# Optimization experiments

Measured on AMD Instinct MI355X. Metric: run time of the kernel, lower is better.

## Reference

```python
import jax, jax.numpy as jnp
import numpy as np

D_MODEL = 512
NUM_HEADS = 8
DEPTH = D_MODEL // NUM_HEADS


def setup_inputs() -> dict:
    key = jax.random.key(0)
    ks = jax.random.split(key, 11)
    B, S = 2, 4096
    scale = 1.0 / np.sqrt(D_MODEL)
    inp = {
        "q": jax.random.normal(ks[0], (B, S, D_MODEL), jnp.float32),
        "k": jax.random.normal(ks[1], (B, S, D_MODEL), jnp.float32),
        "v": jax.random.normal(ks[2], (B, S, D_MODEL), jnp.float32),
        "wq_w": jax.random.normal(ks[3], (D_MODEL, D_MODEL), jnp.float32) * scale,
        "wq_b": jnp.zeros((D_MODEL,), jnp.float32),
        "wk_w": jax.random.normal(ks[4], (D_MODEL, D_MODEL), jnp.float32) * scale,
        "wk_b": jnp.zeros((D_MODEL,), jnp.float32),
        "wv_w": jax.random.normal(ks[5], (D_MODEL, D_MODEL), jnp.float32) * scale,
        "wv_b": jnp.zeros((D_MODEL,), jnp.float32),
        "wo_w": jax.random.normal(ks[6], (D_MODEL, D_MODEL), jnp.float32) * scale,
        "wo_b": jnp.zeros((D_MODEL,), jnp.float32),
    }
    return inp


def _split_heads(x):
    # [B, S, D] -> [B, H, S, depth]
    B, S, _ = x.shape
    return x.reshape(B, S, NUM_HEADS, DEPTH).transpose(0, 2, 1, 3)


def reference(q, k, v, wq_w, wq_b, wk_w, wk_b, wv_w, wv_b, wo_w, wo_b):
    B, S, _ = q.shape
    qh = _split_heads(q @ wq_w.T + wq_b)  # [B,H,S,d]
    kh = _split_heads(k @ wk_w.T + wk_b)
    vh = _split_heads(v @ wv_w.T + wv_b)
    logits = jnp.einsum('bhqd,bhkd->bhqk', qh, kh) / jnp.sqrt(
        jnp.asarray(DEPTH, jnp.float32))
    attn = jax.nn.softmax(logits, axis=-1)
    out = jnp.einsum('bhqk,bhkd->bhqd', attn, vh)  # [B,H,S,d]
    out = out.transpose(0, 2, 1, 3).reshape(B, S, D_MODEL)
    return out @ wo_w.T + wo_b
```

## Files before the change

kernel.cpp:

```cpp
#include <hip/hip_runtime.h>

typedef __attribute__((ext_vector_type(8))) short short8;
typedef __attribute__((ext_vector_type(4))) float float4v;

#define D_MODEL 512
#define NUM_HEADS 8
#define DEPTH 64
#define SEQ 4096
#define BATCH 2
#define MROWS 8192
#define WSZ (D_MODEL * D_MODEL)
#define SCALE_Q 0.18033688011112043f

#define SW(r, c) (((r) * 64) + ((((c) ^ ((r) & 7))) * 8))

static __device__ __forceinline__ unsigned short f2bf(float f) {
  unsigned int u = __builtin_bit_cast(unsigned int, f);
  u += 0x7FFFu + ((u >> 16) & 1u);
  return (unsigned short)(u >> 16);
}
static __device__ __forceinline__ unsigned int pk2(float a, float b) {
  return (unsigned int)f2bf(a) | ((unsigned int)f2bf(b) << 16);
}
static __device__ __forceinline__ unsigned int pk2f(float a, float b) {
  unsigned int ua = __builtin_bit_cast(unsigned int, a) + 0x8000u;
  unsigned int ub = __builtin_bit_cast(unsigned int, b) + 0x8000u;
  return __builtin_amdgcn_perm(ub, ua, 0x07060302u);
}
static __device__ __forceinline__ short8 cvt8(const float* p) {
  float4v f0 = *(const float4v*)p;
  float4v f1 = *(const float4v*)(p + 4);
  short8 s;
#pragma unroll
  for (int j = 0; j < 4; ++j) {
    s[j] = (short)f2bf(f0[j]);
    s[4 + j] = (short)f2bf(f1[j]);
  }
  return s;
}

__global__ __launch_bounds__(256) void cvt3(const float* __restrict__ w0,
                                            const float* __restrict__ w1,
                                            const float* __restrict__ w2,
                                            unsigned short* __restrict__ dst) {
  const float* srcs[3] = {w0, w1, w2};
  const int z = blockIdx.y;
  const float4v* s = (const float4v*)srcs[z];
  uint2* d = (uint2*)(dst + (size_t)z * WSZ);
  int i = blockIdx.x * 256 + threadIdx.x;
  float4v f = s[i];
  d[i] = make_uint2(pk2(f[0], f[1]), pk2(f[2], f[3]));
}
__global__ __launch_bounds__(256) void cvt1(const float* __restrict__ w,
                                            unsigned short* __restrict__ dst) {
  int i = blockIdx.x * 256 + threadIdx.x;
  float4v f = ((const float4v*)w)[i];
  ((uint2*)dst)[i] = make_uint2(pk2(f[0], f[1]), pk2(f[2], f[3]));
}

struct QkvB {
  const float* X[3];
  const float* bias[3];
  unsigned short* out[3];
};
__global__ __launch_bounds__(256, 2) void qkv_fulln(QkvB a,
                                                    const unsigned short* __restrict__ Wall) {
  __shared__ unsigned short Xs[64 * 64];
  __shared__ unsigned short Ws[512 * 64];
  const int z = blockIdx.y;
  const float* __restrict__ X = a.X[z];
  const unsigned short* __restrict__ W = Wall + (size_t)z * WSZ;
  const float* __restrict__ bias = a.bias[z];
  unsigned short* __restrict__ out = a.out[z];
  const int t = threadIdx.x;
  const int w = t >> 6, l = t & 63, lq = l >> 4, lm = l & 15;
  const int mBase = blockIdx.x * 64;
  float4v acc[4][8] = {};

  for (int kc = 0; kc < D_MODEL; kc += 64) {
    __syncthreads();
#pragma unroll
    for (int p = 0; p < 2; ++p) {
      int i = p * 256 + t, r = i >> 3, c = i & 7;
      *(short8*)&Xs[SW(r, c)] = cvt8(&X[(size_t)(mBase + r) * D_MODEL + kc + c * 8]);
    }
#pragma unroll 4
    for (int p = 0; p < 16; ++p) {
      int i = p * 256 + t, r = i >> 3, c = i & 7;
      *(short8*)&Ws[SW(r, c)] = *(const short8*)&W[(size_t)r * D_MODEL + kc + c * 8];
    }
    __syncthreads();
#pragma unroll
    for (int kk = 0; kk < 2; ++kk) {
      short8 av[4];
#pragma unroll
      for (int fm = 0; fm < 4; ++fm)
        av[fm] = *(const short8*)&Xs[SW(fm * 16 + lm, kk * 4 + lq)];
#pragma unroll
      for (int fn = 0; fn < 8; ++fn) {
        short8 bv = *(const short8*)&Ws[SW(w * 128 + fn * 16 + lm, kk * 4 + lq)];
#pragma unroll
        for (int fm = 0; fm < 4; ++fm)
          acc[fm][fn] = __builtin_amdgcn_mfma_f32_16x16x32_bf16(av[fm], bv, acc[fm][fn], 0, 0, 0);
      }
    }
  }
  const int bb = mBase >> 12, s0 = mBase & 4095;
  if (z == 2) {
    __syncthreads();
    unsigned short* T = Ws;
#pragma unroll
    for (int fn = 0; fn < 8; ++fn) {
      int n = w * 128 + fn * 16 + lm;
      float bv = bias[n];
#pragma unroll
      for (int fm = 0; fm < 4; ++fm) {
        int m0 = fm * 16 + lq * 4;
        uint2 u;
        u.x = pk2(acc[fm][fn][0] + bv, acc[fm][fn][1] + bv);
        u.y = pk2(acc[fm][fn][2] + bv, acc[fm][fn][3] + bv);
        *(uint2*)&T[SW(n, m0 >> 3) + (lq & 1) * 4] = u;
      }
    }
    __syncthreads();
#pragma unroll
    for (int p = 0; p < 16; ++p) {
      int i = p * 256 + t, n = i >> 3, cm = i & 7;
      int h = n >> 6, d = n & 63;
      *(short8*)&out[(((size_t)(bb * NUM_HEADS + h) * DEPTH + d) << 12) + s0 + cm * 8] =
          *(const short8*)&T[SW(n, cm)];
    }
  } else {
    const float scale = (z == 0) ? SCALE_Q : 1.0f;
#pragma unroll
    for (int fn = 0; fn < 8; ++fn) {
      int gn = w * 128 + fn * 16 + lm;
      float bv = bias[gn];
      int h = gn >> 6, d = gn & 63;
#pragma unroll
      for (int fm = 0; fm < 4; ++fm) {
#pragma unroll
        for (int r = 0; r < 4; ++r) {
          int s = s0 + fm * 16 + lq * 4 + r;
          out[(((size_t)(bb * NUM_HEADS + h) * SEQ + s) << 6) + d] =
              f2bf((acc[fm][fn][r] + bv) * scale);
        }
      }
    }
  }
}

__global__ __launch_bounds__(256) void gemm_out_128x64(
    const unsigned short* __restrict__ X,
    const unsigned short* __restrict__ W,
    const float* __restrict__ bias,
    float* __restrict__ out) {
  __shared__ unsigned short As[128 * 64];
  __shared__ unsigned short Bs[64 * 64];
  const int t = threadIdx.x;
  const int w = t >> 6, l = t & 63, lq = l >> 4, lm = l & 15;
  const int mq = w * 32;
  const int mBase = blockIdx.x * 128, nBase = blockIdx.y * 64;
  float4v acc[2][4] = {};
  for (int kc = 0; kc < D_MODEL; kc += 64) {
    __syncthreads();
#pragma unroll
    for (int p = 0; p < 4; ++p) {
      int i = p * 256 + t, r = i >> 3, c = i & 7;
      *(short8*)&As[SW(r, c)] = *(const short8*)&X[(size_t)(mBase + r) * D_MODEL + kc + c * 8];
    }
#pragma unroll
    for (int p = 0; p < 2; ++p) {
      int i = p * 256 + t, r = i >> 3, c = i & 7;
      *(short8*)&Bs[SW(r, c)] = *(const short8*)&W[(size_t)(nBase + r) * D_MODEL + kc + c * 8];
    }
    __syncthreads();
#pragma unroll
    for (int kk = 0; kk < 2; ++kk) {
      short8 av[2];
#pragma unroll
      for (int fm = 0; fm < 2; ++fm)
        av[fm] = *(const short8*)&As[SW(mq + fm * 16 + lm, kk * 4 + lq)];
#pragma unroll
      for (int fn = 0; fn < 4; ++fn) {
        short8 bv = *(const short8*)&Bs[SW(fn * 16 + lm, kk * 4 + lq)];
#pragma unroll
        for (int fm = 0; fm < 2; ++fm)
          acc[fm][fn] = __builtin_amdgcn_mfma_f32_16x16x32_bf16(av[fm], bv, acc[fm][fn], 0, 0, 0);
      }
    }
  }
#pragma unroll
  for (int fn = 0; fn < 4; ++fn) {
    int gn = nBase + fn * 16 + lm;
    float bv = bias[gn];
#pragma unroll
    for (int fm = 0; fm < 2; ++fm) {
#pragma unroll
      for (int r = 0; r < 4; ++r) {
        int gm = mBase + mq + fm * 16 + lq * 4 + r;
        out[(size_t)gm * D_MODEL + gn] = acc[fm][fn][r] + bv;
      }
    }
  }
}

__global__ __launch_bounds__(256, 4) void attn(
    const unsigned short* __restrict__ Qh,
    const unsigned short* __restrict__ Kh,
    const unsigned short* __restrict__ Vt,
    unsigned short* __restrict__ AO)
{
  __shared__ unsigned short Ksub[2][64 * 64];
  __shared__ unsigned short Vsub[2][64 * 64];
  __shared__ unsigned short Psub[64 * 64];
  const int t = threadIdx.x;
  const int w = t >> 6;
  const int l = t & 63, lq = l >> 4, lm = l & 15;
  const int bh = blockIdx.y;
  const size_t base = (size_t)bh * SEQ * DEPTH;
  const int qbase = blockIdx.x * 64 + w * 16;
  const unsigned short* __restrict__ Kp = Kh + base;
  const unsigned short* __restrict__ Vp = Vt + base;

  short8 qf[2];
#pragma unroll
  for (int kk = 0; kk < 2; ++kk)
    qf[kk] = *(const short8*)&Qh[base + (size_t)(qbase + lm) * DEPTH + kk * 32 + lq * 8];

  short8 ones;
#pragma unroll
  for (int j = 0; j < 8; ++j) ones[j] = (short)0x3F80;

  float4v oacc[4] = {};
  float4v sumacc = {};
  short8 kreg[2], vreg[2];

#pragma unroll
  for (int p = 0; p < 2; ++p) {
    int i = p * 256 + t, r = i >> 3, c = i & 7;
    kreg[p] = *(const short8*)&Kp[(size_t)r * DEPTH + c * 8];
    vreg[p] = *(const short8*)&Vp[(size_t)r * SEQ + c * 8];
  }
#pragma unroll
  for (int p = 0; p < 2; ++p) {
    int i = p * 256 + t, r = i >> 3, c = i & 7;
    *(short8*)&Ksub[0][SW(r, c)] = kreg[p];
    *(short8*)&Vsub[0][SW(r, c)] = vreg[p];
  }
  __syncthreads();

  auto step = [&](int cur, int tile, bool pf) {
    if (pf) {
      const int s0n = (tile + 1) * 64;
#pragma unroll
      for (int p = 0; p < 2; ++p) {
        int i = p * 256 + t, r = i >> 3, c = i & 7;
        kreg[p] = *(const short8*)&Kp[(size_t)(s0n + r) * DEPTH + c * 8];
        vreg[p] = *(const short8*)&Vp[(size_t)r * SEQ + s0n + c * 8];
      }
    }
#pragma unroll
    for (int f = 0; f < 4; ++f) {
      float4v sacc = {};
#pragma unroll
      for (int kk = 0; kk < 2; ++kk) {
        short8 a = *(const short8*)&Ksub[cur][SW(f * 16 + lm, kk * 4 + lq)];
        sacc = __builtin_amdgcn_mfma_f32_16x16x32_bf16(a, qf[kk], sacc, 0, 0, 0);
      }
      uint2 u;
      u.x = pk2f(__builtin_amdgcn_exp2f(sacc[0]), __builtin_amdgcn_exp2f(sacc[1]));
      u.y = pk2f(__builtin_amdgcn_exp2f(sacc[2]), __builtin_amdgcn_exp2f(sacc[3]));
      *(uint2*)&Psub[SW(w * 16 + lm, 2 * f + (lq >> 1)) + (lq & 1) * 4] = u;
    }
#pragma unroll
    for (int kk = 0; kk < 2; ++kk) {
      short8 a0 = *(const short8*)&Psub[SW(w * 16 + lm, kk * 4 + lq)];
      sumacc = __builtin_amdgcn_mfma_f32_16x16x32_bf16(a0, ones, sumacc, 0, 0, 0);
#pragma unroll
      for (int df = 0; df < 4; ++df) {
        short8 b = *(const short8*)&Vsub[cur][SW(df * 16 + lm, kk * 4 + lq)];
        oacc[df] = __builtin_amdgcn_mfma_f32_16x16x32_bf16(a0, b, oacc[df], 0, 0, 0);
      }
    }
    if (pf) {
#pragma unroll
      for (int p = 0; p < 2; ++p) {
        int i = p * 256 + t, r = i >> 3, c = i & 7;
        *(short8*)&Ksub[cur ^ 1][SW(r, c)] = kreg[p];
        *(short8*)&Vsub[cur ^ 1][SW(r, c)] = vreg[p];
      }
    }
    __syncthreads();
  };

  for (int it = 0; it < 64; it += 2) {
    step(0, it, true);
    step(1, it + 1, it + 2 < 64);
  }

  const int bb = bh >> 3, h = bh & 7;
#pragma unroll
  for (int r = 0; r < 4; ++r) {
    float rinv = 1.0f / sumacc[r];
    int s = qbase + lq * 4 + r;
#pragma unroll
    for (int df = 0; df < 4; ++df) {
      int d = df * 16 + lm;
      AO[((size_t)(bb * SEQ + s)) * D_MODEL + h * DEPTH + d] = f2bf(oacc[df][r] * rinv);
    }
  }
}

extern "C" void kernel_launch(void* const* d_in, const int* in_sizes, int n_in,
                              void* d_out, int out_size, void* d_ws, size_t ws_size,
                              hipStream_t stream) {
  const float* q = (const float*)d_in[0];
  const float* k = (const float*)d_in[1];
  const float* v = (const float*)d_in[2];
  const float* wq = (const float*)d_in[3];
  const float* bq = (const float*)d_in[4];
  const float* wk = (const float*)d_in[5];
  const float* bk = (const float*)d_in[6];
  const float* wv = (const float*)d_in[7];
  const float* bv = (const float*)d_in[8];
  const float* wo = (const float*)d_in[9];
  const float* bo = (const float*)d_in[10];

  const size_t HSD = (size_t)BATCH * NUM_HEADS * SEQ * DEPTH;
  unsigned short* ws = (unsigned short*)d_ws;
  unsigned short* Qh = ws;
  unsigned short* Kh = Qh + HSD;
  unsigned short* Vt = Kh + HSD;
  unsigned short* AO = Vt + HSD;
  unsigned short* Wqkv = AO;
  unsigned short* Wo = Vt;

  cvt3<<<dim3(WSZ / 4 / 256, 3), 256, 0, stream>>>(wq, wk, wv, Wqkv);

  QkvB qa;
  qa.X[0] = q; qa.X[1] = k; qa.X[2] = v;
  qa.bias[0] = bq; qa.bias[1] = bk; qa.bias[2] = bv;
  qa.out[0] = Qh; qa.out[1] = Kh; qa.out[2] = Vt;
  qkv_fulln<<<dim3(MROWS / 64, 3), 256, 0, stream>>>(qa, Wqkv);

  attn<<<dim3(SEQ / 64, BATCH * NUM_HEADS), 256, 0, stream>>>(Qh, Kh, Vt, AO);

  cvt1<<<WSZ / 4 / 256, 256, 0, stream>>>(wo, Wo);

  gemm_out_128x64<<<dim3(MROWS / 128, D_MODEL / 64), 256, 0, stream>>>(AO, Wo, bo, (float*)d_out);
}
```

Before: 246.5 us.

## Split attention keys across waves with register-resident P and LDS reduction

Restructures the attention kernel so each wave handles all 64 queries of the block but only a 16-key slice of each tile. K and V fragments are loaded straight from global memory into registers with double buffering, and the exp'd scores feed the 16x16x16 MFMA directly from registers. This removes the per-tile LDS staging of K, V and P and the per-tile barriers. The cost is a final cross-wave reduction of partial outputs and sums through LDS, higher register pressure (occupancy hint lowered to 2), and uncoalesced 8-byte global loads of V rows with a stride of SEQ.

```diff
diff --git a/kernel.cpp b/kernel.cpp
--- a/kernel.cpp
+++ b/kernel.cpp
@@ -1,6 +1,7 @@
 #include <hip/hip_runtime.h>
 
 typedef __attribute__((ext_vector_type(8))) short short8;
+typedef __attribute__((ext_vector_type(4))) short bf16x4;
 typedef __attribute__((ext_vector_type(4))) float float4v;
 
 #define D_MODEL 512
@@ -205,110 +206,100 @@
   }
 }
 
-__global__ __launch_bounds__(256, 4) void attn(
+__global__ __launch_bounds__(256, 2) void attn(
     const unsigned short* __restrict__ Qh,
     const unsigned short* __restrict__ Kh,
     const unsigned short* __restrict__ Vt,
     unsigned short* __restrict__ AO)
 {
-  __shared__ unsigned short Ksub[2][64 * 64];
-  __shared__ unsigned short Vsub[2][64 * 64];
-  __shared__ unsigned short Psub[64 * 64];
+  __shared__ float Red[4][64 * 65];
+  __shared__ float RedS[4][64];
   const int t = threadIdx.x;
   const int w = t >> 6;
   const int l = t & 63, lq = l >> 4, lm = l & 15;
   const int bh = blockIdx.y;
   const size_t base = (size_t)bh * SEQ * DEPTH;
-  const int qbase = blockIdx.x * 64 + w * 16;
-  const unsigned short* __restrict__ Kp = Kh + base;
-  const unsigned short* __restrict__ Vp = Vt + base;
-
-  short8 qf[2];
-#pragma unroll
-  for (int kk = 0; kk < 2; ++kk)
-    qf[kk] = *(const short8*)&Qh[base + (size_t)(qbase + lm) * DEPTH + kk * 32 + lq * 8];
-
-  short8 ones;
-#pragma unroll
-  for (int j = 0; j < 8; ++j) ones[j] = (short)0x3F80;
-
-  float4v oacc[4] = {};
-  float4v sumacc = {};
-  short8 kreg[2], vreg[2];
-
-#pragma unroll
-  for (int p = 0; p < 2; ++p) {
-    int i = p * 256 + t, r = i >> 3, c = i & 7;
-    kreg[p] = *(const short8*)&Kp[(size_t)r * DEPTH + c * 8];
-    vreg[p] = *(const short8*)&Vp[(size_t)r * SEQ + c * 8];
-  }
-#pragma unroll
-  for (int p = 0; p < 2; ++p) {
-    int i = p * 256 + t, r = i >> 3, c = i & 7;
-    *(short8*)&Ksub[0][SW(r, c)] = kreg[p];
-    *(short8*)&Vsub[0][SW(r, c)] = vreg[p];
-  }
-  __syncthreads();
-
-  auto step = [&](int cur, int tile, bool pf) {
-    if (pf) {
-      const int s0n = (tile + 1) * 64;
-#pragma unroll
-      for (int p = 0; p < 2; ++p) {
-        int i = p * 256 + t, r = i >> 3, c = i & 7;
-        kreg[p] = *(const short8*)&Kp[(size_t)(s0n + r) * DEPTH + c * 8];
-        vreg[p] = *(const short8*)&Vp[(size_t)r * SEQ + s0n + c * 8];
-      }
-    }
-#pragma unroll
-    for (int f = 0; f < 4; ++f) {
+  const int qbase = blockIdx.x * 64;
+  const unsigned short* __restrict__ Kp =
+      Kh + base + (size_t)(w * 16 + lm) * DEPTH;
+  const unsigned short* __restrict__ vrow =
+      Vt + base + (size_t)lm * SEQ + w * 16 + lq * 4;
+
+  short8 qf[4][2];
+#pragma unroll
+  for (int qt = 0; qt < 4; ++qt)
+#pragma unroll
+    for (int kk = 0; kk < 2; ++kk)
+      qf[qt][kk] = *(const short8*)&Qh[base + (size_t)(qbase + qt * 16 + lm) * DEPTH + kk * 32 + lq * 8];
+
+  bf16x4 ones4;
+#pragma unroll
+  for (int j = 0; j < 4; ++j) ones4[j] = (short)0x3F80;
+
+  float4v oacc[4][4] = {};
+  float4v sumacc[4] = {};
+
+  auto prefetch = [&](short8* kf, bf16x4* vf, int tl) {
+    const unsigned short* kp2 = Kp + (size_t)tl * (64 * DEPTH);
+    const unsigned short* vp2 = vrow + tl * 64;
+#pragma unroll
+    for (int kk = 0; kk < 2; ++kk)
+      kf[kk] = *(const short8*)&kp2[kk * 32 + lq * 8];
+#pragma unroll
+    for (int dt = 0; dt < 4; ++dt)
+      vf[dt] = *(const bf16x4*)&vp2[dt * 16 * SEQ];
+  };
+  auto compute = [&](const short8* kf, const bf16x4* vf) {
+#pragma unroll
+    for (int qt = 0; qt < 4; ++qt) {
       float4v sacc = {};
-#pragma unroll
-      for (int kk = 0; kk < 2; ++kk) {
-        short8 a = *(const short8*)&Ksub[cur][SW(f * 16 + lm, kk * 4 + lq)];
-        sacc = __builtin_amdgcn_mfma_f32_16x16x32_bf16(a, qf[kk], sacc, 0, 0, 0);
-      }
+      sacc = __builtin_amdgcn_mfma_f32_16x16x32_bf16(kf[0], qf[qt][0], sacc, 0, 0, 0);
+      sacc = __builtin_amdgcn_mfma_f32_16x16x32_bf16(kf[1], qf[qt][1], sacc, 0, 0, 0);
       uint2 u;
       u.x = pk2f(__builtin_amdgcn_exp2f(sacc[0]), __builtin_amdgcn_exp2f(sacc[1]));
       u.y = pk2f(__builtin_amdgcn_exp2f(sacc[2]), __builtin_amdgcn_exp2f(sacc[3]));
-      *(uint2*)&Psub[SW(w * 16 + lm, 2 * f + (lq >> 1)) + (lq & 1) * 4] = u;
-    }
-#pragma unroll
-    for (int kk = 0; kk < 2; ++kk) {
-      short8 a0 = *(const short8*)&Psub[SW(w * 16 + lm, kk * 4 + lq)];
-      sumacc = __builtin_amdgcn_mfma_f32_16x16x32_bf16(a0, ones, sumacc, 0, 0, 0);
-#pragma unroll
-      for (int df = 0; df < 4; ++df) {
-        short8 b = *(const short8*)&Vsub[cur][SW(df * 16 + lm, kk * 4 + lq)];
-        oacc[df] = __builtin_amdgcn_mfma_f32_16x16x32_bf16(a0, b, oacc[df], 0, 0, 0);
-      }
-    }
-    if (pf) {
-#pragma unroll
-      for (int p = 0; p < 2; ++p) {
-        int i = p * 256 + t, r = i >> 3, c = i & 7;
-        *(short8*)&Ksub[cur ^ 1][SW(r, c)] = kreg[p];
-        *(short8*)&Vsub[cur ^ 1][SW(r, c)] = vreg[p];
-      }
-    }
-    __syncthreads();
+      bf16x4 pa = __builtin_bit_cast(bf16x4, u);
+      sumacc[qt] = __builtin_amdgcn_mfma_f32_16x16x16bf16_1k(pa, ones4, sumacc[qt], 0, 0, 0);
+#pragma unroll
+      for (int dt = 0; dt < 4; ++dt)
+        oacc[qt][dt] = __builtin_amdgcn_mfma_f32_16x16x16bf16_1k(pa, vf[dt], oacc[qt][dt], 0, 0, 0);
+    }
   };
 
-  for (int it = 0; it < 64; it += 2) {
-    step(0, it, true);
-    step(1, it + 1, it + 2 < 64);
-  }
-
+  short8 kfA[2], kfB[2];
+  bf16x4 vfA[4], vfB[4];
+  prefetch(kfA, vfA, 0);
+  for (int tile = 0; tile < 64; tile += 2) {
+    prefetch(kfB, vfB, tile + 1);
+    compute(kfA, vfA);
+    if (tile + 2 < 64) prefetch(kfA, vfA, tile + 2);
+    compute(kfB, vfB);
+  }
+
+#pragma unroll
+  for (int qt = 0; qt < 4; ++qt)
+#pragma unroll
+    for (int dt = 0; dt < 4; ++dt)
+#pragma unroll
+      for (int r = 0; r < 4; ++r)
+        Red[w][(qt * 16 + lq * 4 + r) * 65 + dt * 16 + lm] = oacc[qt][dt][r];
+  if (lm == 0) {
+#pragma unroll
+    for (int qt = 0; qt < 4; ++qt)
+#pragma unroll
+      for (int r = 0; r < 4; ++r)
+        RedS[w][qt * 16 + lq * 4 + r] = sumacc[qt][r];
+  }
+  __syncthreads();
   const int bb = bh >> 3, h = bh & 7;
-#pragma unroll
-  for (int r = 0; r < 4; ++r) {
-    float rinv = 1.0f / sumacc[r];
-    int s = qbase + lq * 4 + r;
-#pragma unroll
-    for (int df = 0; df < 4; ++df) {
-      int d = df * 16 + lm;
-      AO[((size_t)(bb * SEQ + s)) * D_MODEL + h * DEPTH + d] = f2bf(oacc[df][r] * rinv);
-    }
+#pragma unroll 4
+  for (int qq = 0; qq < 16; ++qq) {
+    int q = w * 16 + qq;
+    float s = RedS[0][q] + RedS[1][q] + RedS[2][q] + RedS[3][q];
+    float rinv = 1.0f / s;
+    float a = Red[0][q * 65 + l] + Red[1][q * 65 + l] +
+              Red[2][q * 65 + l] + Red[3][q * 65 + l];
+    AO[((size_t)(bb * SEQ + qbase + q)) * D_MODEL + h * DEPTH + l] = f2bf(a * rinv);
   }
 }
 
```

Result: slower. 318.1 us (+29.0%).

## Keep softmax P in registers by splitting keys across waves with cross-wave reduction

Applied to the files above, without the earlier changes.

The attention kernel now has each wave handle 16 keys of every 64-key tile for all 64 queries, instead of 16 queries over all keys. The S accumulator layout then feeds directly as the A operand of 16x16x16 bf16 MFMAs, so the P tile no longer round-trips through shared memory. Partial outputs and row sums are combined across the four waves through LDS at the end. This costs more registers (16 output accumulators per lane, with occupancy lowered to 2) and uses smaller MFMA shapes, plus a final reduction step.

```diff
diff --git a/kernel.cpp b/kernel.cpp
--- a/kernel.cpp
+++ b/kernel.cpp
@@ -1,6 +1,7 @@
 #include <hip/hip_runtime.h>
 
 typedef __attribute__((ext_vector_type(8))) short short8;
+typedef __attribute__((ext_vector_type(4))) short bf16x4;
 typedef __attribute__((ext_vector_type(4))) float float4v;
 
 #define D_MODEL 512
@@ -205,7 +206,7 @@
   }
 }
 
-__global__ __launch_bounds__(256, 4) void attn(
+__global__ __launch_bounds__(256, 2) void attn(
     const unsigned short* __restrict__ Qh,
     const unsigned short* __restrict__ Kh,
     const unsigned short* __restrict__ Vt,
@@ -213,27 +214,29 @@
 {
   __shared__ unsigned short Ksub[2][64 * 64];
   __shared__ unsigned short Vsub[2][64 * 64];
-  __shared__ unsigned short Psub[64 * 64];
+  __shared__ float RedS[4][64];
   const int t = threadIdx.x;
   const int w = t >> 6;
   const int l = t & 63, lq = l >> 4, lm = l & 15;
   const int bh = blockIdx.y;
   const size_t base = (size_t)bh * SEQ * DEPTH;
-  const int qbase = blockIdx.x * 64 + w * 16;
+  const int qbase = blockIdx.x * 64;
   const unsigned short* __restrict__ Kp = Kh + base;
   const unsigned short* __restrict__ Vp = Vt + base;
 
-  short8 qf[2];
-#pragma unroll
-  for (int kk = 0; kk < 2; ++kk)
-    qf[kk] = *(const short8*)&Qh[base + (size_t)(qbase + lm) * DEPTH + kk * 32 + lq * 8];
-
-  short8 ones;
-#pragma unroll
-  for (int j = 0; j < 8; ++j) ones[j] = (short)0x3F80;
-
-  float4v oacc[4] = {};
-  float4v sumacc = {};
+  short8 qf[4][2];
+#pragma unroll
+  for (int qt = 0; qt < 4; ++qt)
+#pragma unroll
+    for (int kk = 0; kk < 2; ++kk)
+      qf[qt][kk] = *(const short8*)&Qh[base + (size_t)(qbase + qt * 16 + lm) * DEPTH + kk * 32 + lq * 8];
+
+  bf16x4 ones4;
+#pragma unroll
+  for (int j = 0; j < 4; ++j) ones4[j] = (short)0x3F80;
+
+  float4v oacc[4][4] = {};
+  float4v sum4[4] = {};
   short8 kreg[2], vreg[2];
 
 #pragma unroll
@@ -250,6 +253,8 @@
   }
   __syncthreads();
 
+  const int vchunk = w * 2 + (lq >> 1), voff = (lq & 1) * 4;
+
   auto step = [&](int cur, int tile, bool pf) {
     if (pf) {
       const int s0n = (tile + 1) * 64;
@@ -260,28 +265,25 @@
         vreg[p] = *(const short8*)&Vp[(size_t)r * SEQ + s0n + c * 8];
       }
     }
-#pragma unroll
-    for (int f = 0; f < 4; ++f) {
+    short8 kf0 = *(const short8*)&Ksub[cur][SW(w * 16 + lm, lq)];
+    short8 kf1 = *(const short8*)&Ksub[cur][SW(w * 16 + lm, 4 + lq)];
+    bf16x4 vf[4];
+#pragma unroll
+    for (int dt = 0; dt < 4; ++dt)
+      vf[dt] = *(const bf16x4*)&Vsub[cur][SW(dt * 16 + lm, vchunk) + voff];
+#pragma unroll
+    for (int qt = 0; qt < 4; ++qt) {
       float4v sacc = {};
-#pragma unroll
-      for (int kk = 0; kk < 2; ++kk) {
-        short8 a = *(const short8*)&Ksub[cur][SW(f * 16 + lm, kk * 4 + lq)];
-        sacc = __builtin_amdgcn_mfma_f32_16x16x32_bf16(a, qf[kk], sacc, 0, 0, 0);
-      }
+      sacc = __builtin_amdgcn_mfma_f32_16x16x32_bf16(kf0, qf[qt][0], sacc, 0, 0, 0);
+      sacc = __builtin_amdgcn_mfma_f32_16x16x32_bf16(kf1, qf[qt][1], sacc, 0, 0, 0);
       uint2 u;
       u.x = pk2f(__builtin_amdgcn_exp2f(sacc[0]), __builtin_amdgcn_exp2f(sacc[1]));
       u.y = pk2f(__builtin_amdgcn_exp2f(sacc[2]), __builtin_amdgcn_exp2f(sacc[3]));
-      *(uint2*)&Psub[SW(w * 16 + lm, 2 * f + (lq >> 1)) + (lq & 1) * 4] = u;
-    }
-#pragma unroll
-    for (int kk = 0; kk < 2; ++kk) {
-      short8 a0 = *(const short8*)&Psub[SW(w * 16 + lm, kk * 4 + lq)];
-      sumacc = __builtin_amdgcn_mfma_f32_16x16x32_bf16(a0, ones, sumacc, 0, 0, 0);
-#pragma unroll
-      for (int df = 0; df < 4; ++df) {
-        short8 b = *(const short8*)&Vsub[cur][SW(df * 16 + lm, kk * 4 + lq)];
-        oacc[df] = __builtin_amdgcn_mfma_f32_16x16x32_bf16(a0, b, oacc[df], 0, 0, 0);
-      }
+      bf16x4 pa = __builtin_bit_cast(bf16x4, u);
+      sum4[qt] = __builtin_amdgcn_mfma_f32_16x16x16bf16_1k(pa, ones4, sum4[qt], 0, 0, 0);
+#pragma unroll
+      for (int dt = 0; dt < 4; ++dt)
+        oacc[qt][dt] = __builtin_amdgcn_mfma_f32_16x16x16bf16_1k(pa, vf[dt], oacc[qt][dt], 0, 0, 0);
     }
     if (pf) {
 #pragma unroll
@@ -299,16 +301,38 @@
     step(1, it + 1, it + 2 < 64);
   }
 
+  if (lm == 0) {
+#pragma unroll
+    for (int qt = 0; qt < 4; ++qt)
+#pragma unroll
+      for (int r = 0; r < 4; ++r)
+        RedS[w][qt * 16 + lq * 4 + r] = sum4[qt][r];
+  }
+  float* Red = (float*)&Ksub[0][0];
   const int bb = bh >> 3, h = bh & 7;
-#pragma unroll
-  for (int r = 0; r < 4; ++r) {
-    float rinv = 1.0f / sumacc[r];
-    int s = qbase + lq * 4 + r;
-#pragma unroll
-    for (int df = 0; df < 4; ++df) {
-      int d = df * 16 + lm;
-      AO[((size_t)(bb * SEQ + s)) * D_MODEL + h * DEPTH + d] = f2bf(oacc[df][r] * rinv);
-    }
+  const int rq = t >> 2, rd4 = (t & 3) * 4;
+#pragma unroll
+  for (int dt = 0; dt < 4; ++dt) {
+#pragma unroll
+    for (int qt = 0; qt < 4; ++qt)
+#pragma unroll
+      for (int r = 0; r < 4; ++r)
+        Red[w * 1024 + (qt * 16 + lq * 4 + r) * 16 + lm] = oacc[qt][dt][r];
+    __syncthreads();
+    float s = RedS[0][rq] + RedS[1][rq] + RedS[2][rq] + RedS[3][rq];
+    float rinv = 1.0f / s;
+    float4v a0 = *(const float4v*)&Red[rq * 16 + rd4];
+    float4v a1 = *(const float4v*)&Red[1024 + rq * 16 + rd4];
+    float4v a2 = *(const float4v*)&Red[2048 + rq * 16 + rd4];
+    float4v a3 = *(const float4v*)&Red[3072 + rq * 16 + rd4];
+    float4v a;
+#pragma unroll
+    for (int j = 0; j < 4; ++j) a[j] = (a0[j] + a1[j]) + (a2[j] + a3[j]);
+    uint2 u;
+    u.x = pk2(a[0] * rinv, a[1] * rinv);
+    u.y = pk2(a[2] * rinv, a[3] * rinv);
+    *(uint2*)&AO[((size_t)(bb * SEQ + qbase + rq)) * D_MODEL + h * DEPTH + dt * 16 + rd4] = u;
+    __syncthreads();
   }
 }
 
```

Measured after the change: 246.1 us. About the same (-0.2%).
